# Kernel optimization log

Measured on AMD Instinct MI355X. Metric: run time of the kernel, lower is better.

Reference implementation:

```python
import jax, jax.numpy as jnp
import numpy as np

N, M, C, L, T = 1024, 64, 512, 64, 8192
EPS = 1e-16


def setup_inputs() -> dict:
    key = jax.random.key(0)
    ks = jax.random.split(key, 9)
    sc = 0.05
    return {
        "sequence": jax.random.uniform(ks[0], (T, L), dtype=jnp.float32),
        "Wc": jax.random.normal(ks[1], (L + M, C), jnp.float32) * sc,
        "bc": jnp.zeros((C,), jnp.float32),
        "Wr": jax.random.normal(ks[2], (C, M + 6), jnp.float32) * sc,
        "br": jnp.zeros((M + 6,), jnp.float32),
        "Ww": jax.random.normal(ks[3], (C, 3 * M + 6), jnp.float32) * sc,
        "bw": jnp.zeros((3 * M + 6,), jnp.float32),
        "Wo": jax.random.normal(ks[4], (M, L), jnp.float32) * sc,
        "bo": jnp.zeros((L,), jnp.float32),
    }


def _address(Mt, k, beta, g, sh, gamma, w_prev):
    # content addressing: cosine similarity of key against each memory row
    sim = (Mt @ k) / (jnp.linalg.norm(Mt, axis=1) * jnp.linalg.norm(k) + EPS)
    wc = jax.nn.softmax(beta * sim)                      # [N]
    wg = g * wc + (1.0 - g) * w_prev                     # interpolation
    # circular convolution with 3-tap shift kernel (-1, 0, +1)
    ws = sh[0] * jnp.roll(wg, 1) + sh[1] * wg + sh[2] * jnp.roll(wg, -1)
    wsh = ws ** gamma                                    # sharpening
    return wsh / (jnp.sum(wsh) + EPS)


def _head_params(o):
    k = jnp.tanh(o[:M])
    beta = jax.nn.softplus(o[M])
    g = jax.nn.sigmoid(o[M + 1])
    sh = jax.nn.softmax(o[M + 2:M + 5])
    gamma = 1.0 + jax.nn.softplus(o[M + 5])
    return k, beta, g, sh, gamma


def reference(sequence, Wc, bc, Wr, br, Ww, bw, Wo, bo):
    M0 = jnp.full((N, M), 1e-06, jnp.float32)            # memory_bias
    w0 = jnp.zeros((N,), jnp.float32).at[N // 2].set(1.0)  # weight_bias
    r0 = jnp.full((M,), 1e-06, jnp.float32)              # read_bias

    def step(carry, s):
        Mt, ww, rw, r = carry
        h = jnp.tanh(jnp.concatenate([s, r]) @ Wc + bc)  # controller
        # write head: k, beta, g, shift, gamma, erase, add
        ow = h @ Ww + bw
        k, beta, g, sh, gamma = _head_params(ow)
        e = jax.nn.sigmoid(ow[M + 6:2 * M + 6])
        a = jnp.tanh(ow[2 * M + 6:])
        ww_n = _address(Mt, k, beta, g, sh, gamma, ww)
        Mt = Mt * (1.0 - ww_n[:, None] * e[None, :]) + ww_n[:, None] * a[None, :]
        # read head
        orr = h @ Wr + br
        k, beta, g, sh, gamma = _head_params(orr)
        rw_n = _address(Mt, k, beta, g, sh, gamma, rw)
        r_n = rw_n @ Mt                                  # [M]
        s_out = jnp.clip(r_n @ Wo + bo, 0.0, 1.0)
        return (Mt, ww_n, rw_n, r_n), (s_out, ww_n, rw_n, a, r_n)

    _, (seq_out, ww_h, rw_h, a_h, r_h) = jax.lax.scan(step, (M0, w0, w0, r0), sequence)
    return seq_out, ww_h, rw_h, a_h, r_h
```

## Files before the change

### kernel.cpp

```cpp
#include <hip/hip_runtime.h>
#include <math.h>

#define NN 1024
#define MM 64
#define CC 512
#define LL 64
#define TT 8192
#define EPSF 1e-16f

#define OFF_SEQ 0
#define OFF_WW  (TT*LL)
#define OFF_RW  (OFF_WW + TT*NN)
#define OFF_A   (OFF_RW + TT*NN)
#define OFF_R   (OFF_A + TT*MM)

#define WSF_PRE   0
#define WSF_M     (TT*CC)
#define WSF_WCAT  (WSF_M + 32768)

#define BAR() asm volatile("s_waitcnt lgkmcnt(0)\n\ts_barrier" ::: "memory")

__device__ __forceinline__ float sigmoid_f(float x) { return 1.0f / (1.0f + __expf(-x)); }
__device__ __forceinline__ float softplus_f(float x) { return (x > 15.0f) ? x : __logf(1.0f + __expf(x)); }
__device__ __forceinline__ float tanh_f(float x) { float e = __expf(2.0f * x); return 1.0f - 2.0f / (e + 1.0f); }
__device__ __forceinline__ float pow_f(float b, float g) { return __expf(g * __logf(b)); }
__device__ __forceinline__ int bitrev4(int l) {
    return ((l & 1) << 3) | ((l & 2) << 1) | ((l & 4) >> 1) | ((l & 8) >> 3);
}

__device__ __forceinline__ float xor_any(float v, const int m, const int lane) {
    if (m == 1)
        return __int_as_float(__builtin_amdgcn_mov_dpp(__float_as_int(v), 0xB1, 0xF, 0xF, true));
    if (m == 2)
        return __int_as_float(__builtin_amdgcn_mov_dpp(__float_as_int(v), 0x4E, 0xF, 0xF, true));
    return __shfl_xor(v, m, 64);
}

__device__ __forceinline__ float bfly64(float s, const int lane) {
    s += xor_any(s, 1, lane);
    s += xor_any(s, 2, lane);
    s += xor_any(s, 4, lane);
    s += xor_any(s, 8, lane);
    s += xor_any(s, 16, lane);
    s += xor_any(s, 32, lane);
    return s;
}

__global__ void pre_kernel(const float* __restrict__ seq, const float* __restrict__ Wc,
                           const float* __restrict__ bc, float* __restrict__ pre) {
    int gid = blockIdx.x * blockDim.x + threadIdx.x;
    int t = gid >> 9;
    int j = gid & 511;
    if (t >= TT) return;
    const float* s = seq + t * LL;
    float acc = bc[j];
    #pragma unroll 8
    for (int i = 0; i < LL; ++i) acc += s[i] * Wc[i * CC + j];
    pre[gid] = acc;
}

__global__ void pack_kernel(const float* __restrict__ Ww, const float* __restrict__ Wr,
                            float* __restrict__ Wcat) {
    int gid = blockIdx.x * 256 + threadIdx.x;
    if (gid >= 512 * 272) return;
    int r = gid / 272, c = gid - r * 272;
    float v = 0.0f;
    if (c < 198) v = Ww[r * 198 + c];
    else if (c < 268) v = Wr[r * 70 + (c - 198)];
    Wcat[gid] = v;
}

#define WOT_S 68
__global__ __launch_bounds__(1024)
void ntm_kernel(
    const float* __restrict__ pre,
    const float* __restrict__ Wc,
    const float* __restrict__ Wcat,
    const float* __restrict__ br,
    const float* __restrict__ bw,
    const float* __restrict__ Wo,
    const float* __restrict__ bo,
    float* __restrict__ out)
{
    __shared__ __align__(16) float sh_part[4096];
    __shared__ __align__(16) float sh_h[CC];
    __shared__ __align__(16) float sh_kw[MM];
    __shared__ __align__(16) float sh_kr[MM];
    __shared__ __align__(16) float sh_e[MM];
    __shared__ __align__(16) float sh_a[MM];
    __shared__ __align__(16) float sh_scal[16];
    __shared__ __align__(16) float sh_evbuf[NN];
    __shared__ __align__(16) float sh_wpbuf[NN];
    __shared__ __align__(16) float red[4][16];
    __shared__ __align__(16) float wmat[16][MM];
    __shared__ __align__(16) float sh_r[MM];
    __shared__ __align__(16) float sh_WoT[LL * WOT_S];
    __shared__ __align__(16) float sh_bo[LL];
    __shared__ __align__(16) float sh_bw[200];
    __shared__ __align__(16) float sh_br[72];
    __shared__ __align__(16) float sh_pren[CC];

    const int tid  = threadIdx.x;
    const int lane = tid & 63;
    const int wv   = tid >> 6;

    for (int idx = tid; idx < MM * LL; idx += NN) {
        int i = idx >> 6, o = idx & 63;
        sh_WoT[o * WOT_S + i] = Wo[i * LL + o];
    }
    if (tid < LL)  sh_bo[tid] = bo[tid];
    if (tid < 198) sh_bw[tid] = bw[tid];
    if (tid < 70)  sh_br[tid] = br[tid];
    if (tid < MM)  sh_r[tid] = 1e-6f;
    if (tid < CC)  sh_pren[tid] = pre[tid];

    float Mlo[32];
    #pragma unroll
    for (int j = 0; j < 32; ++j) Mlo[j] = 1e-6f;
    float4 mh[8];
    #pragma unroll
    for (int k = 0; k < 8; ++k) mh[k] = make_float4(1e-6f, 1e-6f, 1e-6f, 1e-6f);
    float rown = sqrtf(64.0f * 1e-12f);
    float wwprev = (tid == NN / 2) ? 1.0f : 0.0f;
    float rwprev = wwprev;
    __syncthreads();

    for (int t = 0; t < TT; ++t) {
        {
            int g = tid & 127, q = tid >> 7;
            const float4* wbase = (const float4*)(Wc + (64 + q * 8) * CC) + g;
            float4 ra = *(const float4*)(sh_r + q * 8);
            float4 rb = *(const float4*)(sh_r + q * 8 + 4);
            float rv[8] = {ra.x, ra.y, ra.z, ra.w, rb.x, rb.y, rb.z, rb.w};
            float4 acc = make_float4(0.0f, 0.0f, 0.0f, 0.0f);
            #pragma unroll
            for (int i = 0; i < 8; ++i) {
                float4 w = wbase[i * 128];
                acc.x += rv[i] * w.x; acc.y += rv[i] * w.y;
                acc.z += rv[i] * w.z; acc.w += rv[i] * w.w;
            }
            ((float4*)sh_part)[q * 128 + g] = acc;
        }
        BAR();
        if (tid < CC) {
            float p0 = sh_part[tid]          + sh_part[512 + tid];
            float p1 = sh_part[1024 + tid]   + sh_part[1536 + tid];
            float p2 = sh_part[2048 + tid]   + sh_part[2560 + tid];
            float p3 = sh_part[3072 + tid]   + sh_part[3584 + tid];
            float v = sh_pren[tid] + ((p0 + p1) + (p2 + p3));
            sh_h[tid] = tanh_f(v);
        }
        BAR();
        if (tid < 544) {
            int g = tid % 68, q = tid / 68;
            const float4* wbase = (const float4*)(Wcat + (q * 64) * 272) + g;
            const float4* h4p = (const float4*)(sh_h + q * 64);
            float4 acc = make_float4(0.0f, 0.0f, 0.0f, 0.0f);
            #pragma unroll 2
            for (int i4 = 0; i4 < 16; ++i4) {
                float4 h4 = h4p[i4];
                const float4* wr = wbase + (i4 * 4) * 68;
                float4 w0 = wr[0];
                float4 w1 = wr[68];
                float4 w2 = wr[136];
                float4 w3 = wr[204];
                acc.x += h4.x * w0.x; acc.y += h4.x * w0.y; acc.z += h4.x * w0.z; acc.w += h4.x * w0.w;
                acc.x += h4.y * w1.x; acc.y += h4.y * w1.y; acc.z += h4.y * w1.z; acc.w += h4.y * w1.w;
                acc.x += h4.z * w2.x; acc.y += h4.z * w2.y; acc.z += h4.z * w2.z; acc.w += h4.z * w2.w;
                acc.x += h4.w * w3.x; acc.y += h4.w * w3.y; acc.z += h4.w * w3.z; acc.w += h4.w * w3.w;
            }
            ((float4*)sh_part)[q * 68 + g] = acc;
        }
        BAR();
        float pren_v = 0.0f;
        #define OWV(c) ( (((sh_part[(c)] + sh_part[272 + (c)]) + (sh_part[544 + (c)] + sh_part[816 + (c)])) \
                        + ((sh_part[1088 + (c)] + sh_part[1360 + (c)]) + (sh_part[1632 + (c)] + sh_part[1904 + (c)]))) \
                        + ((c) < 198 ? sh_bw[(c)] : sh_br[(c) - 198]) )
        if (wv == 0) {
            float v = tanh_f(OWV(lane));
            sh_kw[lane] = v;
            float s2 = bfly64(v * v, lane);
            if (lane == 0) sh_scal[6] = sqrtf(s2);
        } else if (wv == 1) {
            float v = tanh_f(OWV(198 + lane));
            sh_kr[lane] = v;
            float s2 = bfly64(v * v, lane);
            if (lane == 0) sh_scal[14] = sqrtf(s2);
        } else if (wv == 2) {
            sh_e[lane] = sigmoid_f(OWV(70 + lane));
        } else if (wv == 3) {
            float v = tanh_f(OWV(134 + lane));
            sh_a[lane] = v;
            out[OFF_A + t * MM + lane] = v;
        } else if (wv == 4) {
            if (lane == 0) {
                sh_scal[0] = softplus_f(OWV(64));
                sh_scal[1] = sigmoid_f(OWV(65));
                float x0 = OWV(66), x1 = OWV(67), x2 = OWV(68);
                float mx = fmaxf(x0, fmaxf(x1, x2));
                float e0 = __expf(x0 - mx), e1 = __expf(x1 - mx), e2 = __expf(x2 - mx);
                float ss = e0 + e1 + e2;
                sh_scal[2] = e0 / ss; sh_scal[3] = e1 / ss; sh_scal[4] = e2 / ss;
                sh_scal[5] = 1.0f + softplus_f(OWV(69));
            }
        } else if (wv == 5) {
            if (lane == 0) {
                sh_scal[8] = softplus_f(OWV(198 + 64));
                sh_scal[9] = sigmoid_f(OWV(198 + 65));
                float x0 = OWV(198 + 66), x1 = OWV(198 + 67), x2 = OWV(198 + 68);
                float mx = fmaxf(x0, fmaxf(x1, x2));
                float e0 = __expf(x0 - mx), e1 = __expf(x1 - mx), e2 = __expf(x2 - mx);
                float ss = e0 + e1 + e2;
                sh_scal[10] = e0 / ss; sh_scal[11] = e1 / ss; sh_scal[12] = e2 / ss;
                sh_scal[13] = 1.0f + softplus_f(OWV(198 + 69));
            }
        } else if (wv >= 6 && wv < 14) {
            if (t + 1 < TT) pren_v = pre[(t + 1) * CC + (tid - 384)];
        } else if (wv == 15) {
            if (t > 0) {
                const float4* r4p = (const float4*)sh_r;
                const float4* wop = (const float4*)(sh_WoT + lane * WOT_S);
                float a0 = 0.0f, a1 = 0.0f;
                #pragma unroll
                for (int i4 = 0; i4 < 16; ++i4) {
                    float4 r = r4p[i4];
                    float4 w = wop[i4];
                    a0 += r.x * w.x + r.y * w.y;
                    a1 += r.z * w.z + r.w * w.w;
                }
                float acc = sh_bo[lane] + a0 + a1;
                out[OFF_SEQ + (t - 1) * LL + lane] = fminf(fmaxf(acc, 0.0f), 1.0f);
            }
        }
        #undef OWV
        BAR();

        float betaW = sh_scal[0], gW = sh_scal[1];
        float s0W = sh_scal[2], s1W = sh_scal[3], s2W = sh_scal[4];
        float gamW = sh_scal[5], knW = sh_scal[6];
        {
            const float4* k4 = (const float4*)sh_kw;
            float d0 = 0.0f, d1 = 0.0f, d2 = 0.0f, d3 = 0.0f;
            #pragma unroll
            for (int j4 = 0; j4 < 8; ++j4) {
                float4 k = k4[j4];
                d0 += Mlo[4*j4]   * k.x;
                d1 += Mlo[4*j4+1] * k.y;
                d2 += Mlo[4*j4+2] * k.z;
                d3 += Mlo[4*j4+3] * k.w;
            }
            #pragma unroll
            for (int k8 = 0; k8 < 8; ++k8) {
                float4 k = k4[8 + k8];
                d0 += mh[k8].x * k.x;
                d1 += mh[k8].y * k.y;
                d2 += mh[k8].z * k.z;
                d3 += mh[k8].w * k.w;
            }
            float dot = (d0 + d1) + (d2 + d3);
            float sim = dot / (rown * knW + EPSF);
            float ev = __expf(betaW * sim);
            sh_evbuf[tid] = ev;
            sh_wpbuf[tid] = wwprev;
            float s = bfly64(ev, lane);
            if (lane == 0) red[0][wv] = s;
        }
        BAR();
        float wshW;
        {
            const float4* rp = (const float4*)red[0];
            float Sev = 0.0f;
            #pragma unroll
            for (int w4 = 0; w4 < 4; ++w4) { float4 p = rp[w4]; Sev += p.x + p.y + p.z + p.w; }
            int tm1 = (tid + NN - 1) & (NN - 1), tp1 = (tid + 1) & (NN - 1);
            float cEV = s0W * sh_evbuf[tm1] + s1W * sh_evbuf[tid] + s2W * sh_evbuf[tp1];
            float cWP = s0W * sh_wpbuf[tm1] + s1W * sh_wpbuf[tid] + s2W * sh_wpbuf[tp1];
            float ws = (gW / Sev) * cEV + (1.0f - gW) * cWP;
            wshW = pow_f(ws, gamW);
            float s = bfly64(wshW, lane);
            if (lane == 0) red[1][wv] = s;
        }
        BAR();
        {
            const float4* rp = (const float4*)red[1];
            float Swsh = 0.0f;
            #pragma unroll
            for (int w4 = 0; w4 < 4; ++w4) { float4 p = rp[w4]; Swsh += p.x + p.y + p.z + p.w; }
            float wwn = wshW / (Swsh + EPSF);
            out[OFF_WW + t * NN + tid] = wwn;
            wwprev = wwn;
            const float4* e4p = (const float4*)sh_e;
            const float4* a4p = (const float4*)sh_a;
            float n0 = 0.0f, n1 = 0.0f, n2 = 0.0f, n3 = 0.0f;
            #pragma unroll
            for (int j4 = 0; j4 < 8; ++j4) {
                float4 e = e4p[j4], a = a4p[j4];
                float m0 = Mlo[4*j4]   * (1.0f - wwn * e.x) + wwn * a.x;
                float m1 = Mlo[4*j4+1] * (1.0f - wwn * e.y) + wwn * a.y;
                float m2 = Mlo[4*j4+2] * (1.0f - wwn * e.z) + wwn * a.z;
                float m3 = Mlo[4*j4+3] * (1.0f - wwn * e.w) + wwn * a.w;
                Mlo[4*j4] = m0; Mlo[4*j4+1] = m1; Mlo[4*j4+2] = m2; Mlo[4*j4+3] = m3;
                n0 += m0 * m0; n1 += m1 * m1; n2 += m2 * m2; n3 += m3 * m3;
            }
            #pragma unroll
            for (int k = 0; k < 8; ++k) {
                float4 e = e4p[8 + k], a = a4p[8 + k];
                float4 m = mh[k];
                m.x = m.x * (1.0f - wwn * e.x) + wwn * a.x;
                m.y = m.y * (1.0f - wwn * e.y) + wwn * a.y;
                m.z = m.z * (1.0f - wwn * e.z) + wwn * a.z;
                m.w = m.w * (1.0f - wwn * e.w) + wwn * a.w;
                mh[k] = m;
                n0 += m.x * m.x; n1 += m.y * m.y; n2 += m.z * m.z; n3 += m.w * m.w;
            }
            rown = sqrtf((n0 + n1) + (n2 + n3));
        }

        float betaR = sh_scal[8], gR = sh_scal[9];
        float s0R = sh_scal[10], s1R = sh_scal[11], s2R = sh_scal[12];
        float gamR = sh_scal[13], knR = sh_scal[14];
        {
            const float4* k4 = (const float4*)sh_kr;
            float d0 = 0.0f, d1 = 0.0f, d2 = 0.0f, d3 = 0.0f;
            #pragma unroll
            for (int j4 = 0; j4 < 8; ++j4) {
                float4 k = k4[j4];
                d0 += Mlo[4*j4]   * k.x;
                d1 += Mlo[4*j4+1] * k.y;
                d2 += Mlo[4*j4+2] * k.z;
                d3 += Mlo[4*j4+3] * k.w;
            }
            #pragma unroll
            for (int k8 = 0; k8 < 8; ++k8) {
                float4 k = k4[8 + k8];
                d0 += mh[k8].x * k.x;
                d1 += mh[k8].y * k.y;
                d2 += mh[k8].z * k.z;
                d3 += mh[k8].w * k.w;
            }
            float dot = (d0 + d1) + (d2 + d3);
            float sim = dot / (rown * knR + EPSF);
            float ev = __expf(betaR * sim);
            sh_evbuf[tid] = ev;
            sh_wpbuf[tid] = rwprev;
            float s = bfly64(ev, lane);
            if (lane == 0) red[2][wv] = s;
        }
        BAR();
        float wshR;
        {
            const float4* rp = (const float4*)red[2];
            float Sev = 0.0f;
            #pragma unroll
            for (int w4 = 0; w4 < 4; ++w4) { float4 p = rp[w4]; Sev += p.x + p.y + p.z + p.w; }
            int tm1 = (tid + NN - 1) & (NN - 1), tp1 = (tid + 1) & (NN - 1);
            float cEV = s0R * sh_evbuf[tm1] + s1R * sh_evbuf[tid] + s2R * sh_evbuf[tp1];
            float cWP = s0R * sh_wpbuf[tm1] + s1R * sh_wpbuf[tid] + s2R * sh_wpbuf[tp1];
            float ws = (gR / Sev) * cEV + (1.0f - gR) * cWP;
            wshR = pow_f(ws, gamR);
            float s = bfly64(wshR, lane);
            if (lane == 0) red[3][wv] = s;
            #pragma unroll
            for (int chunk = 0; chunk < 4; ++chunk) {
                const int cb = chunk * 16;
                float v[16];
                if (chunk < 2) {
                    #pragma unroll
                    for (int i = 0; i < 16; ++i) v[i] = wshR * Mlo[chunk * 16 + i];
                } else {
                    #pragma unroll
                    for (int k = 0; k < 4; ++k) {
                        float4 m = mh[(chunk - 2) * 4 + k];
                        v[4*k]   = wshR * m.x;
                        v[4*k+1] = wshR * m.y;
                        v[4*k+2] = wshR * m.z;
                        v[4*k+3] = wshR * m.w;
                    }
                }
                #pragma unroll
                for (int st = 0; st < 4; ++st) {
                    const int m = 1 << st;
                    const int hs = 8 >> st;
                    bool hi = (lane & m) != 0;
                    #pragma unroll
                    for (int i = 0; i < 8; ++i) {
                        if (i < hs) {
                            float send = hi ? v[i] : v[i + hs];
                            float recv = xor_any(send, m, lane);
                            float keep = hi ? v[i + hs] : v[i];
                            v[i] = keep + recv;
                        }
                    }
                }
                float v0 = v[0];
                v0 += xor_any(v0, 16, lane);
                v0 += xor_any(v0, 32, lane);
                if (lane < 16) wmat[wv][cb + bitrev4(lane)] = v0;
            }
        }
        BAR();
        {
            if (wv >= 6 && wv < 14 && t + 1 < TT) sh_pren[tid - 384] = pren_v;
            const float4* rp = (const float4*)red[3];
            float Swsh = 0.0f;
            #pragma unroll
            for (int w4 = 0; w4 < 4; ++w4) { float4 p = rp[w4]; Swsh += p.x + p.y + p.z + p.w; }
            float inv = 1.0f / (Swsh + EPSF);
            float rwn = wshR * inv;
            out[OFF_RW + t * NN + tid] = rwn;
            rwprev = rwn;
            if (tid < MM) {
                float rv = 0.0f;
                #pragma unroll
                for (int w = 0; w < 16; ++w) rv += wmat[w][tid];
                rv *= inv;
                sh_r[tid] = rv;
                out[OFF_R + t * MM + tid] = rv;
            }
        }
        BAR();
    }

    if (tid < LL) {
        const float4* r4p = (const float4*)sh_r;
        const float4* wop = (const float4*)(sh_WoT + tid * WOT_S);
        float a0 = 0.0f, a1 = 0.0f;
        #pragma unroll
        for (int i4 = 0; i4 < 16; ++i4) {
            float4 r = r4p[i4];
            float4 w = wop[i4];
            a0 += r.x * w.x + r.y * w.y;
            a1 += r.z * w.z + r.w * w.w;
        }
        float acc = sh_bo[tid] + a0 + a1;
        out[OFF_SEQ + (TT - 1) * LL + tid] = fminf(fmaxf(acc, 0.0f), 1.0f);
    }
}

extern "C" void kernel_launch(void* const* d_in, const int* in_sizes, int n_in,
                              void* d_out, int out_size, void* d_ws, size_t ws_size,
                              hipStream_t stream) {
    const float* seq = (const float*)d_in[0];
    const float* Wc  = (const float*)d_in[1];
    const float* bc  = (const float*)d_in[2];
    const float* Wr  = (const float*)d_in[3];
    const float* br  = (const float*)d_in[4];
    const float* Ww  = (const float*)d_in[5];
    const float* bw  = (const float*)d_in[6];
    const float* Wo  = (const float*)d_in[7];
    const float* bo  = (const float*)d_in[8];
    float* out = (float*)d_out;

    float* wsf  = (float*)d_ws;
    float* pre  = wsf + WSF_PRE;
    float* Wcat = wsf + WSF_WCAT;

    pre_kernel<<<(TT * CC) / 256, 256, 0, stream>>>(seq, Wc, bc, pre);
    pack_kernel<<<(512 * 272 + 255) / 256, 256, 0, stream>>>(Ww, Wr, Wcat);
    ntm_kernel<<<1, 1024, 0, stream>>>(pre, Wc, Wcat, br, bw, Wo, bo, out);
}
```

Before: 134.8 ms.

## Use DPP row-shift reductions, interleave shift buffers, move output projection earlier

Replaces the xor butterfly wave reduction, which used ds_swizzle/shfl for strides 4 and up, with a DPP row_shr plus row_bcast15/31 scan whose total ends up in lane 63. This avoids the LDS-permute latency on a reduction that sits on the serial critical path of each step. The ev and previous-weight buffers are packed into one float2 array, so each circular-convolution neighbour needs one LDS load instead of two. The Wo output projection for the previous step moves to wave 15 in the matvec phase, which wave 15 did not use, taking it off the post-matvec phase.

```diff
diff --git a/kernel.cpp b/kernel.cpp
--- a/kernel.cpp
+++ b/kernel.cpp
@@ -36,13 +36,18 @@
     return __shfl_xor(v, m, 64);
 }
 
-__device__ __forceinline__ float bfly64(float s, const int lane) {
-    s += xor_any(s, 1, lane);
-    s += xor_any(s, 2, lane);
-    s += xor_any(s, 4, lane);
-    s += xor_any(s, 8, lane);
-    s += xor_any(s, 16, lane);
-    s += xor_any(s, 32, lane);
+template<int CTRL>
+__device__ __forceinline__ float dpp_add(float s) {
+    int sh = __builtin_amdgcn_update_dpp(0, __float_as_int(s), CTRL, 0xF, 0xF, false);
+    return s + __int_as_float(sh);
+}
+__device__ __forceinline__ float rowsum64(float s) {
+    s = dpp_add<0x111>(s);
+    s = dpp_add<0x112>(s);
+    s = dpp_add<0x114>(s);
+    s = dpp_add<0x118>(s);
+    s = dpp_add<0x142>(s);
+    s = dpp_add<0x143>(s);
     return s;
 }
 
@@ -89,8 +94,7 @@
     __shared__ __align__(16) float sh_e[MM];
     __shared__ __align__(16) float sh_a[MM];
     __shared__ __align__(16) float sh_scal[16];
-    __shared__ __align__(16) float sh_evbuf[NN];
-    __shared__ __align__(16) float sh_wpbuf[NN];
+    __shared__ __align__(16) float2 sh_evwp[NN];
     __shared__ __align__(16) float red[4][16];
     __shared__ __align__(16) float wmat[16][MM];
     __shared__ __align__(16) float sh_r[MM];
@@ -170,6 +174,21 @@
                 acc.x += h4.w * w3.x; acc.y += h4.w * w3.y; acc.z += h4.w * w3.z; acc.w += h4.w * w3.w;
             }
             ((float4*)sh_part)[q * 68 + g] = acc;
+        } else if (wv == 15) {
+            if (t > 0) {
+                const float4* r4p = (const float4*)sh_r;
+                const float4* wop = (const float4*)(sh_WoT + lane * WOT_S);
+                float a0 = 0.0f, a1 = 0.0f;
+                #pragma unroll
+                for (int i4 = 0; i4 < 16; ++i4) {
+                    float4 r = r4p[i4];
+                    float4 w = wop[i4];
+                    a0 += r.x * w.x + r.y * w.y;
+                    a1 += r.z * w.z + r.w * w.w;
+                }
+                float acc = sh_bo[lane] + a0 + a1;
+                out[OFF_SEQ + (t - 1) * LL + lane] = fminf(fmaxf(acc, 0.0f), 1.0f);
+            }
         }
         BAR();
         float pren_v = 0.0f;
@@ -179,13 +198,13 @@
         if (wv == 0) {
             float v = tanh_f(OWV(lane));
             sh_kw[lane] = v;
-            float s2 = bfly64(v * v, lane);
-            if (lane == 0) sh_scal[6] = sqrtf(s2);
+            float s2 = rowsum64(v * v);
+            if (lane == 63) sh_scal[6] = sqrtf(s2);
         } else if (wv == 1) {
             float v = tanh_f(OWV(198 + lane));
             sh_kr[lane] = v;
-            float s2 = bfly64(v * v, lane);
-            if (lane == 0) sh_scal[14] = sqrtf(s2);
+            float s2 = rowsum64(v * v);
+            if (lane == 63) sh_scal[14] = sqrtf(s2);
         } else if (wv == 2) {
             sh_e[lane] = sigmoid_f(OWV(70 + lane));
         } else if (wv == 3) {
@@ -216,21 +235,6 @@
             }
         } else if (wv >= 6 && wv < 14) {
             if (t + 1 < TT) pren_v = pre[(t + 1) * CC + (tid - 384)];
-        } else if (wv == 15) {
-            if (t > 0) {
-                const float4* r4p = (const float4*)sh_r;
-                const float4* wop = (const float4*)(sh_WoT + lane * WOT_S);
-                float a0 = 0.0f, a1 = 0.0f;
-                #pragma unroll
-                for (int i4 = 0; i4 < 16; ++i4) {
-                    float4 r = r4p[i4];
-                    float4 w = wop[i4];
-                    a0 += r.x * w.x + r.y * w.y;
-                    a1 += r.z * w.z + r.w * w.w;
-                }
-                float acc = sh_bo[lane] + a0 + a1;
-                out[OFF_SEQ + (t - 1) * LL + lane] = fminf(fmaxf(acc, 0.0f), 1.0f);
-            }
         }
         #undef OWV
         BAR();
@@ -260,10 +264,9 @@
             float dot = (d0 + d1) + (d2 + d3);
             float sim = dot / (rown * knW + EPSF);
             float ev = __expf(betaW * sim);
-            sh_evbuf[tid] = ev;
-            sh_wpbuf[tid] = wwprev;
-            float s = bfly64(ev, lane);
-            if (lane == 0) red[0][wv] = s;
+            sh_evwp[tid] = make_float2(ev, wwprev);
+            float s = rowsum64(ev);
+            if (lane == 63) red[0][wv] = s;
         }
         BAR();
         float wshW;
@@ -273,12 +276,13 @@
             #pragma unroll
             for (int w4 = 0; w4 < 4; ++w4) { float4 p = rp[w4]; Sev += p.x + p.y + p.z + p.w; }
             int tm1 = (tid + NN - 1) & (NN - 1), tp1 = (tid + 1) & (NN - 1);
-            float cEV = s0W * sh_evbuf[tm1] + s1W * sh_evbuf[tid] + s2W * sh_evbuf[tp1];
-            float cWP = s0W * sh_wpbuf[tm1] + s1W * sh_wpbuf[tid] + s2W * sh_wpbuf[tp1];
+            float2 em1 = sh_evwp[tm1], ec = sh_evwp[tid], ep1 = sh_evwp[tp1];
+            float cEV = s0W * em1.x + s1W * ec.x + s2W * ep1.x;
+            float cWP = s0W * em1.y + s1W * ec.y + s2W * ep1.y;
             float ws = (gW / Sev) * cEV + (1.0f - gW) * cWP;
             wshW = pow_f(ws, gamW);
-            float s = bfly64(wshW, lane);
-            if (lane == 0) red[1][wv] = s;
+            float s = rowsum64(wshW);
+            if (lane == 63) red[1][wv] = s;
         }
         BAR();
         {
@@ -341,10 +345,9 @@
             float dot = (d0 + d1) + (d2 + d3);
             float sim = dot / (rown * knR + EPSF);
             float ev = __expf(betaR * sim);
-            sh_evbuf[tid] = ev;
-            sh_wpbuf[tid] = rwprev;
-            float s = bfly64(ev, lane);
-            if (lane == 0) red[2][wv] = s;
+            sh_evwp[tid] = make_float2(ev, rwprev);
+            float s = rowsum64(ev);
+            if (lane == 63) red[2][wv] = s;
         }
         BAR();
         float wshR;
@@ -354,12 +357,13 @@
             #pragma unroll
             for (int w4 = 0; w4 < 4; ++w4) { float4 p = rp[w4]; Sev += p.x + p.y + p.z + p.w; }
             int tm1 = (tid + NN - 1) & (NN - 1), tp1 = (tid + 1) & (NN - 1);
-            float cEV = s0R * sh_evbuf[tm1] + s1R * sh_evbuf[tid] + s2R * sh_evbuf[tp1];
-            float cWP = s0R * sh_wpbuf[tm1] + s1R * sh_wpbuf[tid] + s2R * sh_wpbuf[tp1];
+            float2 em1 = sh_evwp[tm1], ec = sh_evwp[tid], ep1 = sh_evwp[tp1];
+            float cEV = s0R * em1.x + s1R * ec.x + s2R * ep1.x;
+            float cWP = s0R * em1.y + s1R * ec.y + s2R * ep1.y;
             float ws = (gR / Sev) * cEV + (1.0f - gR) * cWP;
             wshR = pow_f(ws, gamR);
-            float s = bfly64(wshR, lane);
-            if (lane == 0) red[3][wv] = s;
+            float s = rowsum64(wshR);
+            if (lane == 63) red[3][wv] = s;
             #pragma unroll
             for (int chunk = 0; chunk < 4; ++chunk) {
                 const int cb = chunk * 16;
```

Measured after the change: 129.4 ms. 1.04x faster.
